# Performance work log

Hardware: AMD Instinct MI355X
Metric: run time of the kernel (lower is better)

The kernel has to match this reference:

```python
import jax, jax.numpy as jnp
import numpy as np

# Constants derived from configs (see init_kwargs)
NUM_X = 64
NUM_Y = 64
NUM_BINS = 128          # num_lct_bins
NUM_SUB = 10            # num_sub_bins
NUM_V = NUM_SUB * NUM_BINS
PAD = NUM_V             # pad_length
X_MIN, X_MAX = -1.0, 1.0
Y_MIN, Y_MAX = -1.0, 1.0
T_RES = 32e-12
SPEED_OF_LIGHT = 3.0e8
V_RANGE = (SPEED_OF_LIGHT * NUM_BINS * T_RES / 2.0) ** 2
V_BASE_RES = V_RANGE / NUM_V

B, NY, NX = 32, 64, 64


def setup_inputs() -> dict:
    key = jax.random.key(0)
    k1, k2, k3 = jax.random.split(key, 3)
    # wall positions well inside [X_MIN, X_MAX] so clamping is rare but exercised
    cur_pos = jax.random.uniform(k1, (B, NY, NX, 2), minval=-0.9, maxval=0.9, dtype=jnp.float32)
    # small per-frame (x, y, v) shifts
    deltas = jax.random.normal(k2, (B, 3), dtype=jnp.float32) * 0.01
    # stands in for the precomputed parabola-histogram voxel table
    canon_voxel = jax.random.uniform(k3, (NUM_Y, NUM_X, NUM_V + 2 * PAD), dtype=jnp.float32)
    return {"cur_pos": cur_pos, "deltas": deltas, "canon_voxel": canon_voxel, "is_cam_motion": 0}


def reference(cur_pos, deltas, canon_voxel, is_cam_motion):
    batch, n_y, n_x = cur_pos.shape[:3]
    sign = 1.0 if is_cam_motion else -1.0  # cam motion adds deltas, object motion subtracts
    dx = deltas[:, 0][:, None, None]
    dy = deltas[:, 1][:, None, None]
    x_samp = jnp.clip(cur_pos[..., 0] + sign * dx, X_MIN, X_MAX)  # (B, ny, nx)
    y_samp = jnp.clip(cur_pos[..., 1] + sign * dy, Y_MIN, Y_MAX)
    # int() truncation toward zero, as in torch .int()
    x_idx = (NUM_X * (x_samp - X_MIN) / (X_MAX - X_MIN)).astype(jnp.int32)
    y_idx = (NUM_Y * (y_samp - Y_MIN) / (Y_MAX - Y_MIN)).astype(jnp.int32)
    x_idx = jnp.clip(x_idx, 0, NUM_X - 1)
    y_idx = jnp.clip(y_idx, 0, NUM_Y - 1)
    # v axis sampling; note the source always subtracts the v-shift ('or True')
    xlin = jnp.linspace(0.0, V_RANGE, NUM_BINS).astype(cur_pos.dtype)  # (numBins,)
    v_samp = -deltas[:, 2][:, None, None, None] + xlin                 # (B, 1, 1, numBins)
    v_idx = PAD + (v_samp / V_BASE_RES).astype(jnp.int32)
    v_idx = jnp.broadcast_to(v_idx, (batch, n_y, n_x, NUM_BINS))
    # data-dependent gather from the voxel table
    hists = canon_voxel[y_idx[..., None], x_idx[..., None], v_idx]     # (B, ny, nx, numBins)
    return hists
```

## Files before the change

kernel.cpp:

```cpp
#include <hip/hip_runtime.h>

#define NX_ 64
#define NY_ 64
#define NBINS 128
#define NSUB 10
#define NV (NSUB * NBINS)
#define PADL NV
#define ROWLEN (NV + 2 * PADL)
#define BATCH 32
#define NROWS (NY_ * NX_)
#define CELLS (BATCH * NY_ * NX_)
#define CAP 128
#define TABN (BATCH * NBINS)

__global__ __launch_bounds__(256) void bin_kernel(
    const float* __restrict__ cur_pos,
    const float* __restrict__ deltas,
    const int* __restrict__ is_cam,
    const float* __restrict__ voxel,
    int* __restrict__ cnt,
    unsigned* __restrict__ bucket,
    float* __restrict__ out,
    float vr_f, float vbase_f)
{
    int cell = blockIdx.x * 256 + threadIdx.x;
    int b = cell >> 12;

    float sign = (is_cam[0] != 0) ? 1.0f : -1.0f;
    float2 p = ((const float2*)cur_pos)[cell];
    float dx = deltas[b * 3 + 0];
    float dy = deltas[b * 3 + 1];

    float xs = fminf(fmaxf(p.x + sign * dx, -1.0f), 1.0f);
    float ys = fminf(fmaxf(p.y + sign * dy, -1.0f), 1.0f);
    int xi = (int)(32.0f * (xs + 1.0f));
    int yi = (int)(32.0f * (ys + 1.0f));
    xi = min(max(xi, 0), NX_ - 1);
    yi = min(max(yi, 0), NY_ - 1);
    int r = yi * NX_ + xi;

    int pos = atomicAdd(&cnt[r], 1);
    if (pos < CAP) {
        bucket[r * CAP + pos] = (unsigned)cell;
    } else {
        const float* __restrict__ row = voxel + (size_t)r * ROWLEN;
        float* __restrict__ o = out + (size_t)cell * NBINS;
        float dv = deltas[b * 3 + 2];
        float step = vr_f / 127.0f;
        for (int k = 0; k < NBINS; ++k) {
            float xl = (k == NBINS - 1) ? vr_f : (float)k * step;
            int t = PADL + (int)((-dv + xl) / vbase_f);
            o[k] = row[t];
        }
    }
}

__global__ __launch_bounds__(512) void row_gather_kernel(
    const float* __restrict__ voxel,
    const float* __restrict__ deltas,
    const int* __restrict__ cnt,
    const unsigned* __restrict__ bucket,
    float* __restrict__ out,
    float vr_f, float vbase_f)
{
    int r = blockIdx.x;
    int n = cnt[r];
    if (n == 0) return;
    if (n > CAP) n = CAP;

    __shared__ __align__(16) float span[ROWLEN];
    __shared__ int tabl[TABN];
    __shared__ unsigned s_cells[CAP];
    __shared__ int s_lo, s_len;

    int tid = threadIdx.x;

    if (tid < n) s_cells[tid] = bucket[r * CAP + tid];

    float step = vr_f / 127.0f;
    #pragma unroll
    for (int i = tid; i < TABN; i += 512) {
        int b = i >> 7;
        int k = i & (NBINS - 1);
        float dv = deltas[b * 3 + 2];
        float xl = (k == NBINS - 1) ? vr_f : (float)k * step;
        tabl[i] = PADL + (int)((-dv + xl) / vbase_f);
    }
    __syncthreads();

    if (tid < 64) {
        int bb = tid & 31;
        int lo = tabl[bb * 128];
        int hi = tabl[bb * 128 + 127];
        #pragma unroll
        for (int m = 16; m >= 1; m >>= 1) {
            lo = min(lo, __shfl_xor(lo, m));
            hi = max(hi, __shfl_xor(hi, m));
        }
        if (tid == 0) {
            lo = max(lo, 0);
            hi = min(hi, ROWLEN - 1);
            s_lo = lo;
            s_len = hi - lo + 1;
        }
    }
    __syncthreads();

    int lo4 = s_lo & ~3;
    int end4 = (s_lo + s_len + 3) & ~3;
    if (end4 > ROWLEN) end4 = ROWLEN;
    int nvec = (end4 - lo4) >> 2;
    const float4* __restrict__ row4 =
        (const float4*)(voxel + (size_t)r * ROWLEN) + (lo4 >> 2);
    float4* span4 = (float4*)span;
    for (int i = tid; i < nvec; i += 512) span4[i] = row4[i];
    __syncthreads();

    int g = tid >> 5, lane = tid & 31;
    for (int ci = g; ci < n; ci += 16) {
        unsigned cell = s_cells[ci];
        int b = (int)(cell >> 12);
        const int* t = tabl + b * NBINS;
        int i0 = t[lane]      - lo4;
        int i1 = t[lane + 32] - lo4;
        int i2 = t[lane + 64] - lo4;
        int i3 = t[lane + 96] - lo4;
        float v0 = span[i0], v1 = span[i1], v2 = span[i2], v3 = span[i3];
        float* __restrict__ o = out + (size_t)cell * NBINS;
        o[lane]      = v0;
        o[lane + 32] = v1;
        o[lane + 64] = v2;
        o[lane + 96] = v3;
    }
}

extern "C" void kernel_launch(void* const* d_in, const int* in_sizes, int n_in,
                              void* d_out, int out_size, void* d_ws, size_t ws_size,
                              hipStream_t stream) {
    const float* cur_pos = (const float*)d_in[0];
    const float* deltas  = (const float*)d_in[1];
    const float* voxel   = (const float*)d_in[2];
    const int*   is_cam  = (const int*)d_in[3];
    float* out = (float*)d_out;

    int* cnt = (int*)d_ws;
    unsigned* bucket = (unsigned*)(cnt + NROWS);

    const double vr_d = ((3.0e8 * 128.0) * 32e-12 / 2.0) * ((3.0e8 * 128.0) * 32e-12 / 2.0);
    const float vr_f = (float)vr_d;
    const float vbase_f = (float)(vr_d / (double)NV);

    hipMemsetAsync(cnt, 0, NROWS * sizeof(int), stream);

    hipLaunchKernelGGL(bin_kernel, dim3(CELLS / 256), dim3(256), 0, stream,
                       cur_pos, deltas, is_cam, voxel, cnt, bucket, out,
                       vr_f, vbase_f);

    hipLaunchKernelGGL(row_gather_kernel, dim3(NROWS), dim3(512), 0, stream,
                       voxel, deltas, cnt, bucket, out, vr_f, vbase_f);
}
```

Before: 135.8 us.

## Fuse memset, binning and row gather into one cooperative persistent kernel

Replaces the memset plus two kernel launches with a single cooperative kernel of 1024 blocks. Grid-wide syncs separate three phases: clearing counters, binning cells into row buckets, and gathering rows. Each block builds the per-batch v-index table once and reuses it for every row it handles, including the overflow path. This removes launch overhead and repeated table setup, at the cost of two grid barriers and a 1024-block grid that must be fully co-resident given the large shared-memory footprint per block.

```diff
diff --git a/kernel.cpp b/kernel.cpp
--- a/kernel.cpp
+++ b/kernel.cpp
@@ -1,4 +1,7 @@
 #include <hip/hip_runtime.h>
+#include <hip/hip_cooperative_groups.h>
+
+namespace cg = cooperative_groups;
 
 #define NX_ 64
 #define NY_ 64
@@ -12,8 +15,10 @@
 #define CELLS (BATCH * NY_ * NX_)
 #define CAP 128
 #define TABN (BATCH * NBINS)
+#define GRID_ 1024
+#define TPB 512
 
-__global__ __launch_bounds__(256) void bin_kernel(
+__global__ __launch_bounds__(TPB, 8) void fused_kernel(
     const float* __restrict__ cur_pos,
     const float* __restrict__ deltas,
     const int* __restrict__ is_cam,
@@ -23,63 +28,19 @@
     float* __restrict__ out,
     float vr_f, float vbase_f)
 {
-    int cell = blockIdx.x * 256 + threadIdx.x;
-    int b = cell >> 12;
-
-    float sign = (is_cam[0] != 0) ? 1.0f : -1.0f;
-    float2 p = ((const float2*)cur_pos)[cell];
-    float dx = deltas[b * 3 + 0];
-    float dy = deltas[b * 3 + 1];
-
-    float xs = fminf(fmaxf(p.x + sign * dx, -1.0f), 1.0f);
-    float ys = fminf(fmaxf(p.y + sign * dy, -1.0f), 1.0f);
-    int xi = (int)(32.0f * (xs + 1.0f));
-    int yi = (int)(32.0f * (ys + 1.0f));
-    xi = min(max(xi, 0), NX_ - 1);
-    yi = min(max(yi, 0), NY_ - 1);
-    int r = yi * NX_ + xi;
-
-    int pos = atomicAdd(&cnt[r], 1);
-    if (pos < CAP) {
-        bucket[r * CAP + pos] = (unsigned)cell;
-    } else {
-        const float* __restrict__ row = voxel + (size_t)r * ROWLEN;
-        float* __restrict__ o = out + (size_t)cell * NBINS;
-        float dv = deltas[b * 3 + 2];
-        float step = vr_f / 127.0f;
-        for (int k = 0; k < NBINS; ++k) {
-            float xl = (k == NBINS - 1) ? vr_f : (float)k * step;
-            int t = PADL + (int)((-dv + xl) / vbase_f);
-            o[k] = row[t];
-        }
-    }
-}
-
-__global__ __launch_bounds__(512) void row_gather_kernel(
-    const float* __restrict__ voxel,
-    const float* __restrict__ deltas,
-    const int* __restrict__ cnt,
-    const unsigned* __restrict__ bucket,
-    float* __restrict__ out,
-    float vr_f, float vbase_f)
-{
-    int r = blockIdx.x;
-    int n = cnt[r];
-    if (n == 0) return;
-    if (n > CAP) n = CAP;
-
     __shared__ __align__(16) float span[ROWLEN];
     __shared__ int tabl[TABN];
     __shared__ unsigned s_cells[CAP];
-    __shared__ int s_lo, s_len;
+    __shared__ int s_lo, s_hi;
 
+    cg::grid_group gg = cg::this_grid();
     int tid = threadIdx.x;
+    int gtid = blockIdx.x * TPB + tid;
 
-    if (tid < n) s_cells[tid] = bucket[r * CAP + tid];
-
+    if (gtid < NROWS) cnt[gtid] = 0;
     float step = vr_f / 127.0f;
     #pragma unroll
-    for (int i = tid; i < TABN; i += 512) {
+    for (int i = tid; i < TABN; i += TPB) {
         int b = i >> 7;
         int k = i & (NBINS - 1);
         float dv = deltas[b * 3 + 2];
@@ -87,7 +48,6 @@
         tabl[i] = PADL + (int)((-dv + xl) / vbase_f);
     }
     __syncthreads();
-
     if (tid < 64) {
         int bb = tid & 31;
         int lo = tabl[bb * 128];
@@ -98,39 +58,72 @@
             hi = max(hi, __shfl_xor(hi, m));
         }
         if (tid == 0) {
-            lo = max(lo, 0);
-            hi = min(hi, ROWLEN - 1);
-            s_lo = lo;
-            s_len = hi - lo + 1;
+            s_lo = max(lo, 0);
+            s_hi = min(hi, ROWLEN - 1);
         }
     }
-    __syncthreads();
+    gg.sync();
+
+    if (gtid < CELLS) {
+        int cell = gtid;
+        int b = cell >> 12;
+        float sign = (is_cam[0] != 0) ? 1.0f : -1.0f;
+        float2 p = ((const float2*)cur_pos)[cell];
+        float dx = deltas[b * 3 + 0];
+        float dy = deltas[b * 3 + 1];
+        float xs = fminf(fmaxf(p.x + sign * dx, -1.0f), 1.0f);
+        float ys = fminf(fmaxf(p.y + sign * dy, -1.0f), 1.0f);
+        int xi = (int)(32.0f * (xs + 1.0f));
+        int yi = (int)(32.0f * (ys + 1.0f));
+        xi = min(max(xi, 0), NX_ - 1);
+        yi = min(max(yi, 0), NY_ - 1);
+        int r = yi * NX_ + xi;
+        int pos = atomicAdd(&cnt[r], 1);
+        if (pos < CAP) {
+            bucket[r * CAP + pos] = (unsigned)cell;
+        } else {
+            const float* __restrict__ row = voxel + (size_t)r * ROWLEN;
+            float* __restrict__ o = out + (size_t)cell * NBINS;
+            for (int k = 0; k < NBINS; ++k) o[k] = row[tabl[(b << 7) + k]];
+        }
+    }
+    gg.sync();
 
     int lo4 = s_lo & ~3;
-    int end4 = (s_lo + s_len + 3) & ~3;
+    int end4 = (s_hi + 4) & ~3;
     if (end4 > ROWLEN) end4 = ROWLEN;
     int nvec = (end4 - lo4) >> 2;
-    const float4* __restrict__ row4 =
-        (const float4*)(voxel + (size_t)r * ROWLEN) + (lo4 >> 2);
-    float4* span4 = (float4*)span;
-    for (int i = tid; i < nvec; i += 512) span4[i] = row4[i];
-    __syncthreads();
+    int g = tid >> 5, lane = tid & 31;
 
-    int g = tid >> 5, lane = tid & 31;
-    for (int ci = g; ci < n; ci += 16) {
-        unsigned cell = s_cells[ci];
-        int b = (int)(cell >> 12);
-        const int* t = tabl + b * NBINS;
-        int i0 = t[lane]      - lo4;
-        int i1 = t[lane + 32] - lo4;
-        int i2 = t[lane + 64] - lo4;
-        int i3 = t[lane + 96] - lo4;
-        float v0 = span[i0], v1 = span[i1], v2 = span[i2], v3 = span[i3];
-        float* __restrict__ o = out + (size_t)cell * NBINS;
-        o[lane]      = v0;
-        o[lane + 32] = v1;
-        o[lane + 64] = v2;
-        o[lane + 96] = v3;
+    for (int r = blockIdx.x; r < NROWS; r += GRID_) {
+        int n = cnt[r];
+        if (n > CAP) n = CAP;
+        __syncthreads();
+        if (n > 0) {
+            if (tid < n) s_cells[tid] = bucket[r * CAP + tid];
+            const float4* __restrict__ row4 =
+                (const float4*)(voxel + (size_t)r * ROWLEN) + (lo4 >> 2);
+            float4* span4 = (float4*)span;
+            for (int i = tid; i < nvec; i += TPB) span4[i] = row4[i];
+        }
+        __syncthreads();
+        if (n > 0) {
+            for (int ci = g; ci < n; ci += TPB / 32) {
+                unsigned cell = s_cells[ci];
+                int b = (int)(cell >> 12);
+                const int* t = tabl + b * NBINS;
+                int i0 = t[lane]      - lo4;
+                int i1 = t[lane + 32] - lo4;
+                int i2 = t[lane + 64] - lo4;
+                int i3 = t[lane + 96] - lo4;
+                float v0 = span[i0], v1 = span[i1], v2 = span[i2], v3 = span[i3];
+                float* __restrict__ o = out + (size_t)cell * NBINS;
+                o[lane]      = v0;
+                o[lane + 32] = v1;
+                o[lane + 64] = v2;
+                o[lane + 96] = v3;
+            }
+        }
     }
 }
 
@@ -147,15 +140,13 @@
     unsigned* bucket = (unsigned*)(cnt + NROWS);
 
     const double vr_d = ((3.0e8 * 128.0) * 32e-12 / 2.0) * ((3.0e8 * 128.0) * 32e-12 / 2.0);
-    const float vr_f = (float)vr_d;
-    const float vbase_f = (float)(vr_d / (double)NV);
+    float vr_f = (float)vr_d;
+    float vbase_f = (float)(vr_d / (double)NV);
 
-    hipMemsetAsync(cnt, 0, NROWS * sizeof(int), stream);
+    void* args[] = { (void*)&cur_pos, (void*)&deltas, (void*)&is_cam,
+                     (void*)&voxel, (void*)&cnt, (void*)&bucket, (void*)&out,
+                     (void*)&vr_f, (void*)&vbase_f };
 
-    hipLaunchKernelGGL(bin_kernel, dim3(CELLS / 256), dim3(256), 0, stream,
-                       cur_pos, deltas, is_cam, voxel, cnt, bucket, out,
-                       vr_f, vbase_f);
-
-    hipLaunchKernelGGL(row_gather_kernel, dim3(NROWS), dim3(512), 0, stream,
-                       voxel, deltas, cnt, bucket, out, vr_f, vbase_f);
+    hipLaunchCooperativeKernel((const void*)fused_kernel, dim3(GRID_), dim3(TPB),
+                               args, 0, stream);
 }
```

After: 323.8 us. 139% more time.
